# Kernel optimization log

Measured on AMD Instinct MI355X. Metric: run time of the kernel, lower is better.

The kernel has to match this reference:

```python
import jax, jax.numpy as jnp
import numpy as np

N = 100000
D = 128
E = 1600000
L = 3
LN_EPS = 1e-5
SM_EPS = 1e-16  # PyG softmax denominator eps
NEG_SLOPE = 0.2  # GATConv leaky_relu slope


def setup_inputs() -> dict:
    key = jax.random.key(0)
    ks = jax.random.split(key, 9)
    x = jax.random.normal(ks[0], (N, D), dtype=jnp.float32)
    edge_index = jax.random.randint(ks[1], (2, E), 0, N, dtype=jnp.int64)
    # Per-level GATConv params (heads=1, concat -> out dim D)
    W = jax.random.normal(ks[2], (L, D, D), dtype=jnp.float32) / np.sqrt(D)
    att_src = jax.random.normal(ks[3], (L, D), dtype=jnp.float32) / np.sqrt(D)
    att_dst = jax.random.normal(ks[4], (L, D), dtype=jnp.float32) / np.sqrt(D)
    bias = jnp.zeros((L, D), dtype=jnp.float32)
    ln_gamma = jnp.ones((L, D), dtype=jnp.float32)
    ln_beta = jnp.zeros((L, D), dtype=jnp.float32)
    return {"x": x, "edge_index": edge_index, "W": W, "att_src": att_src,
            "att_dst": att_dst, "bias": bias, "ln_gamma": ln_gamma, "ln_beta": ln_beta}


def _gat_level(x, src, dst, W, a_src, a_dst, b):
    h = x @ W                                   # [N, D] transformed features
    alpha_s = h @ a_src                         # [N] per-node src attention logit
    alpha_d = h @ a_dst                         # [N]
    alpha = alpha_s[src] + alpha_d[dst]         # [E'] edge logits
    alpha = jax.nn.leaky_relu(alpha, NEG_SLOPE)
    amax = jax.ops.segment_max(alpha, dst, num_segments=N)  # self-loops guarantee nonempty segments
    alpha = jnp.exp(alpha - amax[dst])
    denom = jax.ops.segment_sum(alpha, dst, num_segments=N)
    alpha = alpha / (denom[dst] + SM_EPS)       # segment softmax over incoming edges
    msg = h[src] * alpha[:, None]               # [E', D]
    out = jax.ops.segment_sum(msg, dst, num_segments=N)
    return out + b


def reference(x, edge_index, W, att_src, att_dst, bias, ln_gamma, ln_beta):
    loops = jnp.arange(N, dtype=edge_index.dtype)
    src = jnp.concatenate([edge_index[0], loops])  # PyG GATConv adds self-loops
    dst = jnp.concatenate([edge_index[1], loops])
    for i in range(L):
        x_att = _gat_level(x, src, dst, W[i], att_src[i], att_dst[i], bias[i])
        y = x + x_att
        mu = jnp.mean(y, axis=-1, keepdims=True)
        var = jnp.mean(jnp.square(y - mu), axis=-1, keepdims=True)
        y = (y - mu) * jax.lax.rsqrt(var + LN_EPS) * ln_gamma[i] + ln_beta[i]
        x = jax.nn.relu(y)  # dropout is identity in eval mode
    return x
```

## Files before the change

kernel.cpp:

```cpp
#include <hip/hip_runtime.h>
#include <hip/hip_fp16.h>
#include <cstdint>

#define D 128
#define NEG_SLOPE 0.2f
#define LN_EPS 1e-5f
#define SM_EPS 1e-16f

typedef _Float16 f16x8 __attribute__((ext_vector_type(8)));
typedef float f32x4 __attribute__((ext_vector_type(4)));


__global__ void hist_dst(const int* __restrict__ dst, int E, int* __restrict__ deg) {
    int e = blockIdx.x * blockDim.x + threadIdx.x;
    if (e < E) atomicAdd(&deg[dst[e]], 1);
}

__global__ void scanA(const int* __restrict__ deg, int n,
                      int* __restrict__ excl, int* __restrict__ bsums) {
    __shared__ int s[256];
    int t = threadIdx.x;
    int v = blockIdx.x * 256 + t;
    int d = (v < n) ? deg[v] : 0;
    s[t] = d;
    __syncthreads();
    for (int off = 1; off < 256; off <<= 1) {
        int tv = (t >= off) ? s[t - off] : 0;
        __syncthreads();
        s[t] += tv;
        __syncthreads();
    }
    if (v < n) excl[v] = s[t] - d;
    if (t == 255) bsums[blockIdx.x] = s[255];
}

__global__ void scanB(int* __restrict__ bsums, int nb) {
    __shared__ int s[512];
    int t = threadIdx.x;
    int v = (t < nb) ? bsums[t] : 0;
    s[t] = v;
    __syncthreads();
    for (int off = 1; off < 512; off <<= 1) {
        int tv = (t >= off) ? s[t - off] : 0;
        __syncthreads();
        s[t] += tv;
        __syncthreads();
    }
    if (t < nb) bsums[t] = s[t] - v;
}

__global__ void scanC(int* __restrict__ rowptr, const int* __restrict__ bsums,
                      int* __restrict__ cursor, int n, int total) {
    int v = blockIdx.x * blockDim.x + threadIdx.x;
    if (v < n) { rowptr[v] += bsums[v >> 8]; cursor[v] = 0; }
    if (v == 0) rowptr[n] = total;
}

__global__ void fill_csr(const int* __restrict__ src, const int* __restrict__ dst,
                         int E, const int* __restrict__ rowptr,
                         int* __restrict__ cursor, int* __restrict__ col) {
    int e = blockIdx.x * blockDim.x + threadIdx.x;
    if (e >= E) return;
    int d = dst[e];
    int p = rowptr[d] + atomicAdd(&cursor[d], 1);
    col[p] = src[e];
}


__global__ void prep_w(const float* __restrict__ W, const float* __restrict__ a_src,
                       const float* __restrict__ a_dst, __half* __restrict__ Wt,
                       float* __restrict__ wsv, float* __restrict__ wdv) {
    int l = blockIdx.x;
    const float* Wl = W + (size_t)l * D * D;
    __half* Wtl = Wt + (size_t)l * D * D;
    int t = threadIdx.x;
    __shared__ float sA[D], sD[D];
    if (t < D) { sA[t] = a_src[l * D + t]; sD[t] = a_dst[l * D + t]; }
    __syncthreads();
    if (t < D) {
        float ps = 0.f, pd = 0.f;
        for (int c = 0; c < D; ++c) {
            float wv = Wl[t * D + c];
            ps += wv * sA[c];
            pd += wv * sD[c];
        }
        wsv[l * D + t] = ps;
        wdv[l * D + t] = pd;
    }
    int c = t & 127, kh = t >> 7;
    for (int g = 0; g < 8; ++g) {
        int k0 = kh * 64 + g * 8;
        union { __half hv[8]; float4 f4; } u;
        #pragma unroll
        for (int rr = 0; rr < 8; ++rr) u.hv[rr] = __float2half(Wl[(k0 + rr) * D + c]);
        *(float4*)(Wtl + (size_t)c * D + k0) = u.f4;
    }
}


__global__ __launch_bounds__(256) void gemm_mfma(
        const float* __restrict__ x, const __half* __restrict__ Wt,
        const float* __restrict__ wsv, const float* __restrict__ wdv,
        __half* __restrict__ h, float* __restrict__ as_, float* __restrict__ ad_, int n) {
    __shared__ char sXa[32768];
    __shared__ char sWb[32768];
    int t = threadIdx.x;
    int row0 = blockIdx.x * 128;
    int lane = t & 63;
    int w = t >> 6;
    int wrow = (w >> 1) * 64;
    int wcol = (w & 1) * 64;

    const float4* xv = (const float4*)x;
    #pragma unroll
    for (int i = 0; i < 16; ++i) {
        int slot = i * 256 + t;
        int r = slot >> 5;
        int c4 = slot & 31;
        int gr = row0 + r;
        float4 v = (gr < n) ? xv[(size_t)gr * 32 + c4] : make_float4(0.f, 0.f, 0.f, 0.f);
        union { __half2 q[2]; float2 f; } u;
        u.q[0] = __floats2half2_rn(v.x, v.y);
        u.q[1] = __floats2half2_rn(v.z, v.w);
        *(float2*)(sXa + r * 256 + ((c4 * 8) ^ ((r & 7) << 4))) = u.f;
    }
    const float4* wv = (const float4*)Wt;
    #pragma unroll
    for (int i = 0; i < 8; ++i) {
        int chunk = i * 256 + t;
        int r = chunk >> 4;
        int c16 = chunk & 15;
        float4 v = wv[chunk];
        *(float4*)(sWb + r * 256 + ((c16 * 16) ^ ((r & 7) << 4))) = v;
    }
    __syncthreads();

    f32x4 acc[4][4];
    #pragma unroll
    for (int a = 0; a < 4; ++a)
        #pragma unroll
        for (int b = 0; b < 4; ++b) acc[a][b] = (f32x4){0.f, 0.f, 0.f, 0.f};

    #pragma unroll
    for (int ks = 0; ks < 4; ++ks) {
        int kbyte = ks * 64 + (lane >> 4) * 16;
        f16x8 aF[4], bF[4];
        #pragma unroll
        for (int tt = 0; tt < 4; ++tt) {
            int ra = wrow + tt * 16 + (lane & 15);
            aF[tt] = *(f16x8*)(sXa + ra * 256 + (kbyte ^ ((ra & 7) << 4)));
            int rb = wcol + tt * 16 + (lane & 15);
            bF[tt] = *(f16x8*)(sWb + rb * 256 + (kbyte ^ ((rb & 7) << 4)));
        }
        #pragma unroll
        for (int tr = 0; tr < 4; ++tr)
            #pragma unroll
            for (int tc = 0; tc < 4; ++tc)
                acc[tr][tc] = __builtin_amdgcn_mfma_f32_16x16x32_f16(aF[tr], bF[tc], acc[tr][tc], 0, 0, 0);
    }

    #pragma unroll
    for (int tr = 0; tr < 4; ++tr) {
        #pragma unroll
        for (int reg = 0; reg < 4; ++reg) {
            int gr = row0 + wrow + tr * 16 + (lane >> 4) * 4 + reg;
            if (gr < n) {
                #pragma unroll
                for (int tc = 0; tc < 4; ++tc) {
                    int gc = wcol + tc * 16 + (lane & 15);
                    h[(size_t)gr * D + gc] = __float2half(acc[tr][tc][reg]);
                }
            }
        }
    }

    int r = t >> 1, hh = t & 1;
    float ps = 0.f, pd = 0.f;
    const float4* s4 = (const float4*)wsv + hh * 16;
    const float4* d4 = (const float4*)wdv + hh * 16;
    #pragma unroll
    for (int g = 0; g < 8; ++g) {
        int kbyte = hh * 128 + g * 16;
        f16x8 xa = *(f16x8*)(sXa + r * 256 + (kbyte ^ ((r & 7) << 4)));
        float4 sa = s4[g * 2], sb = s4[g * 2 + 1];
        float4 da = d4[g * 2], db = d4[g * 2 + 1];
        ps += (float)xa[0] * sa.x + (float)xa[1] * sa.y + (float)xa[2] * sa.z + (float)xa[3] * sa.w
            + (float)xa[4] * sb.x + (float)xa[5] * sb.y + (float)xa[6] * sb.z + (float)xa[7] * sb.w;
        pd += (float)xa[0] * da.x + (float)xa[1] * da.y + (float)xa[2] * da.z + (float)xa[3] * da.w
            + (float)xa[4] * db.x + (float)xa[5] * db.y + (float)xa[6] * db.z + (float)xa[7] * db.w;
    }
    ps += __shfl_xor(ps, 1);
    pd += __shfl_xor(pd, 1);
    if (hh == 0 && row0 + r < n) { as_[row0 + r] = ps; ad_[row0 + r] = pd; }
}


__global__ __launch_bounds__(256) void aggregate(
        const float* __restrict__ xin, const __half* __restrict__ h,
        const float* __restrict__ as_, const float* __restrict__ ad_,
        const int* __restrict__ col, const int* __restrict__ rowptr,
        const float* __restrict__ bias, const float* __restrict__ gamma,
        const float* __restrict__ beta, float* __restrict__ xout, int n) {
    __shared__ int     sS[4][64];
    __shared__ __half2 sW[4][64];
    int tid = threadIdx.x;
    int wslot = tid >> 6;
    int lane = tid & 63;
    int wid = (int)((blockIdx.x * blockDim.x + tid) >> 6);
    if (wid >= n) return;
    int v = wid;
    int grp = lane >> 4;
    int gl  = lane & 15;
    int start = rowptr[v], end = rowptr[v + 1];
    float adv = ad_[v];
    float self_a = as_[v] + adv;
    self_a = (self_a > 0.f) ? self_a : NEG_SLOPE * self_a;

    float mval = self_a;
    int   s0 = 0;
    float a0 = -1e30f;
    for (int cb = start; cb < end; cb += 64) {
        int e = cb + lane;
        int   sl = 0;
        float al = -1e30f;
        if (e < end) {
            sl = col[e];
            float aa = as_[sl] + adv;
            al = (aa > 0.f) ? aa : NEG_SLOPE * aa;
        }
        if (cb == start) { s0 = sl; a0 = al; }
        mval = fmaxf(mval, al);
    }
    #pragma unroll
    for (int d = 32; d >= 1; d >>= 1) mval = fmaxf(mval, __shfl_xor(mval, d));

    float wl = __expf(a0 - mval);
    float sacc = wl;
    sS[wslot][lane] = s0;
    sW[wslot][lane] = __float2half2_rn(wl);

    __half2 hacc[4];
    #pragma unroll
    for (int j = 0; j < 4; ++j) hacc[j] = __float2half2_rn(0.f);

    const float4* h4 = (const float4*)h;

    for (int cb = start; cb < end; cb += 64) {
        if (cb != start) {
            int e = cb + lane;
            int   sl = 0;
            float al = -1e30f;
            if (e < end) {
                sl = col[e];
                float aa = as_[sl] + adv;
                al = (aa > 0.f) ? aa : NEG_SLOPE * aa;
            }
            float wl2 = __expf(al - mval);
            sacc += wl2;
            sS[wslot][lane] = sl;
            sW[wslot][lane] = __float2half2_rn(wl2);
        }
        int cnt = min(64, end - cb);
        for (int i = grp; i < cnt; i += 4) {
            int s = sS[wslot][i];
            __half2 w2 = sW[wslot][i];
            union { float4 f4; __half2 h2[4]; } u;
            u.f4 = h4[(size_t)s * 16 + gl];
            #pragma unroll
            for (int j = 0; j < 4; ++j) hacc[j] = __hfma2(u.h2[j], w2, hacc[j]);
        }
    }
    #pragma unroll
    for (int d = 32; d >= 1; d >>= 1) sacc += __shfl_xor(sacc, d);

    float acc[8];
    #pragma unroll
    for (int j = 0; j < 4; ++j) {
        float2 f = __half22float2(hacc[j]);
        acc[2 * j] = f.x;
        acc[2 * j + 1] = f.y;
    }
    #pragma unroll
    for (int j = 0; j < 8; ++j) {
        acc[j] += __shfl_xor(acc[j], 16);
        acc[j] += __shfl_xor(acc[j], 32);
    }

    float w_self = __expf(self_a - mval);
    sacc += w_self;
    {
        union { float4 f4; __half2 h2[4]; } u;
        u.f4 = h4[(size_t)v * 16 + gl];
        #pragma unroll
        for (int j = 0; j < 4; ++j) {
            float2 f = __half22float2(u.h2[j]);
            acc[2 * j]     += w_self * f.x;
            acc[2 * j + 1] += w_self * f.y;
        }
    }
    float inv = 1.f / (sacc + SM_EPS);

    const float4* xr = (const float4*)(xin + (size_t)v * D) + gl * 2;
    float4 xa = xr[0], xb = xr[1];
    const float4* b4 = (const float4*)bias + gl * 2;
    float4 ba = b4[0], bb = b4[1];
    float y[8];
    y[0] = xa.x + acc[0] * inv + ba.x;
    y[1] = xa.y + acc[1] * inv + ba.y;
    y[2] = xa.z + acc[2] * inv + ba.z;
    y[3] = xa.w + acc[3] * inv + ba.w;
    y[4] = xb.x + acc[4] * inv + bb.x;
    y[5] = xb.y + acc[5] * inv + bb.y;
    y[6] = xb.z + acc[6] * inv + bb.z;
    y[7] = xb.w + acc[7] * inv + bb.w;

    float s2 = 0.f;
    #pragma unroll
    for (int j = 0; j < 8; ++j) s2 += y[j];
    #pragma unroll
    for (int d = 8; d >= 1; d >>= 1) s2 += __shfl_xor(s2, d);
    float mu = s2 * (1.f / 128.f);
    float vs = 0.f;
    #pragma unroll
    for (int j = 0; j < 8; ++j) { float dd = y[j] - mu; vs += dd * dd; }
    #pragma unroll
    for (int d = 8; d >= 1; d >>= 1) vs += __shfl_xor(vs, d);
    float rstd = rsqrtf(vs * (1.f / 128.f) + LN_EPS);

    const float4* g4 = (const float4*)gamma + gl * 2;
    const float4* t4 = (const float4*)beta + gl * 2;
    float4 ga = g4[0], gb = g4[1];
    float4 ta = t4[0], tb = t4[1];
    float4 oa, ob;
    oa.x = fmaxf((y[0] - mu) * rstd * ga.x + ta.x, 0.f);
    oa.y = fmaxf((y[1] - mu) * rstd * ga.y + ta.y, 0.f);
    oa.z = fmaxf((y[2] - mu) * rstd * ga.z + ta.z, 0.f);
    oa.w = fmaxf((y[3] - mu) * rstd * ga.w + ta.w, 0.f);
    ob.x = fmaxf((y[4] - mu) * rstd * gb.x + tb.x, 0.f);
    ob.y = fmaxf((y[5] - mu) * rstd * gb.y + tb.y, 0.f);
    ob.z = fmaxf((y[6] - mu) * rstd * gb.z + tb.z, 0.f);
    ob.w = fmaxf((y[7] - mu) * rstd * gb.w + tb.w, 0.f);

    if (lane < 16) {
        float4* o4 = (float4*)(xout + (size_t)v * D) + gl * 2;
        o4[0] = oa;
        o4[1] = ob;
    }
}


extern "C" void kernel_launch(void* const* d_in, const int* in_sizes, int n_in,
                              void* d_out, int out_size, void* d_ws, size_t ws_size,
                              hipStream_t stream) {
    const float* x       = (const float*)d_in[0];
    const int*   edge    = (const int*)d_in[1];
    const float* W       = (const float*)d_in[2];
    const float* att_src = (const float*)d_in[3];
    const float* att_dst = (const float*)d_in[4];
    const float* bias    = (const float*)d_in[5];
    const float* gamma   = (const float*)d_in[6];
    const float* beta    = (const float*)d_in[7];
    float* out = (float*)d_out;

    const int N = in_sizes[0] / D;
    const int E = in_sizes[1] / 2;

    const int* src = edge;
    const int* dst = edge + E;

    char* ws = (char*)d_ws;
    size_t off = 0;
    auto carve = [&](size_t bytes) -> char* {
        char* p = ws + off;
        off = (off + bytes + 511) & ~(size_t)511;
        return p;
    };
    int*    rowptr = (int*)carve((size_t)(N + 1) * 4);
    int*    cursor = (int*)carve((size_t)N * 4);
    int*    bsums  = (int*)carve(512 * 4);
    int*    col    = (int*)carve((size_t)E * 4);
    __half* h      = (__half*)carve((size_t)N * D * 2);
    float*  as_    = (float*)carve((size_t)N * 4);
    float*  ad_    = (float*)carve((size_t)N * 4);
    float*  x1     = (float*)carve((size_t)N * D * 4);
    __half* Wt     = (__half*)carve((size_t)3 * D * D * 2);
    float*  wsv    = (float*)carve((size_t)3 * D * 4);
    float*  wdv    = (float*)carve((size_t)3 * D * 4);
    (void)ws_size;

    const int TPB = 256;
    int nbN = (N + TPB - 1) / TPB;
    int nbE = (E + TPB - 1) / TPB;

    prep_w<<<3, TPB, 0, stream>>>(W, att_src, att_dst, Wt, wsv, wdv);

    hipMemsetAsync(cursor, 0, (size_t)N * 4, stream);
    hist_dst<<<nbE, TPB, 0, stream>>>(dst, E, cursor);
    scanA<<<nbN, TPB, 0, stream>>>(cursor, N, rowptr, bsums);
    scanB<<<1, 512, 0, stream>>>(bsums, nbN);
    scanC<<<nbN, TPB, 0, stream>>>(rowptr, bsums, cursor, N, E);
    fill_csr<<<nbE, TPB, 0, stream>>>(src, dst, E, rowptr, cursor, col);

    int gemmGrid = (N + 127) / 128;
    int aggGrid  = (N * 64 + TPB - 1) / TPB;

    const float* xin = x;
    float* bufs[3] = { x1, x1, out };
    for (int l = 0; l < 3; ++l) {
        const __half* Wtl = Wt + (size_t)l * D * D;
        const float*  wsl = wsv + (size_t)l * D;
        const float*  wdl = wdv + (size_t)l * D;
        const float*  bl  = bias + (size_t)l * D;
        const float*  gl  = gamma + (size_t)l * D;
        const float*  btl = beta + (size_t)l * D;
        float* xout = bufs[l];

        gemm_mfma<<<gemmGrid, TPB, 0, stream>>>(xin, Wtl, wsl, wdl, h, as_, ad_, N);
        aggregate<<<aggGrid, TPB, 0, stream>>>(xin, h, as_, ad_, col, rowptr,
                                               bl, gl, btl, xout, N);
        xin = xout;
    }
}
```

Baseline: 626.3 us.

## Record per-edge rank in histogram pass and parallelize weight prep

```diff
diff --git a/kernel.cpp b/kernel.cpp
--- a/kernel.cpp
+++ b/kernel.cpp
@@ -11,9 +11,10 @@
 typedef float f32x4 __attribute__((ext_vector_type(4)));
 
 
-__global__ void hist_dst(const int* __restrict__ dst, int E, int* __restrict__ deg) {
+__global__ void hist_dst(const int* __restrict__ dst, int E,
+                         int* __restrict__ deg, int* __restrict__ rank) {
     int e = blockIdx.x * blockDim.x + threadIdx.x;
-    if (e < E) atomicAdd(&deg[dst[e]], 1);
+    if (e < E) rank[e] = atomicAdd(&deg[dst[e]], 1);
 }
 
 __global__ void scanA(const int* __restrict__ deg, int n,
@@ -50,50 +51,63 @@
 }
 
 __global__ void scanC(int* __restrict__ rowptr, const int* __restrict__ bsums,
-                      int* __restrict__ cursor, int n, int total) {
+                      int n, int total) {
     int v = blockIdx.x * blockDim.x + threadIdx.x;
-    if (v < n) { rowptr[v] += bsums[v >> 8]; cursor[v] = 0; }
+    if (v < n) rowptr[v] += bsums[v >> 8];
     if (v == 0) rowptr[n] = total;
 }
 
 __global__ void fill_csr(const int* __restrict__ src, const int* __restrict__ dst,
-                         int E, const int* __restrict__ rowptr,
-                         int* __restrict__ cursor, int* __restrict__ col) {
+                         const int* __restrict__ rank, int E,
+                         const int* __restrict__ rowptr, int* __restrict__ col) {
     int e = blockIdx.x * blockDim.x + threadIdx.x;
     if (e >= E) return;
     int d = dst[e];
-    int p = rowptr[d] + atomicAdd(&cursor[d], 1);
-    col[p] = src[e];
+    int p = rowptr[d] + rank[e];
+    atomicExch(&col[p], src[e]);
 }
 
 
 __global__ void prep_w(const float* __restrict__ W, const float* __restrict__ a_src,
                        const float* __restrict__ a_dst, __half* __restrict__ Wt,
                        float* __restrict__ wsv, float* __restrict__ wdv) {
-    int l = blockIdx.x;
+    int l = blockIdx.x >> 3;
+    int part = blockIdx.x & 7;
     const float* Wl = W + (size_t)l * D * D;
     __half* Wtl = Wt + (size_t)l * D * D;
     int t = threadIdx.x;
-    __shared__ float sA[D], sD[D];
-    if (t < D) { sA[t] = a_src[l * D + t]; sD[t] = a_dst[l * D + t]; }
+    int c0 = part * 16;
+
+    __shared__ float sT[128][17];
+    #pragma unroll
+    for (int i = 0; i < 8; ++i) {
+        int id = i * 256 + t;
+        int k = id >> 4, c = id & 15;
+        sT[k][c] = Wl[(size_t)k * D + c0 + c];
+    }
     __syncthreads();
-    if (t < D) {
-        float ps = 0.f, pd = 0.f;
-        for (int c = 0; c < D; ++c) {
-            float wv = Wl[t * D + c];
-            ps += wv * sA[c];
-            pd += wv * sD[c];
-        }
-        wsv[l * D + t] = ps;
-        wdv[l * D + t] = pd;
-    }
-    int c = t & 127, kh = t >> 7;
-    for (int g = 0; g < 8; ++g) {
-        int k0 = kh * 64 + g * 8;
+    {
+        int c = t >> 4, kg = t & 15;
         union { __half hv[8]; float4 f4; } u;
         #pragma unroll
-        for (int rr = 0; rr < 8; ++rr) u.hv[rr] = __float2half(Wl[(k0 + rr) * D + c]);
-        *(float4*)(Wtl + (size_t)c * D + k0) = u.f4;
+        for (int j = 0; j < 8; ++j) u.hv[j] = __float2half(sT[kg * 8 + j][c]);
+        *(float4*)(Wtl + (size_t)(c0 + c) * D + kg * 8) = u.f4;
+    }
+
+    if (part == 0) {
+        __shared__ float sA[D], sD[D];
+        if (t < D) { sA[t] = a_src[l * D + t]; sD[t] = a_dst[l * D + t]; }
+        __syncthreads();
+        if (t < D) {
+            float ps = 0.f, pd = 0.f;
+            for (int c = 0; c < D; ++c) {
+                float wv = Wl[(size_t)t * D + c];
+                ps += wv * sA[c];
+                pd += wv * sD[c];
+            }
+            wsv[l * D + t] = ps;
+            wdv[l * D + t] = pd;
+        }
     }
 }
 
@@ -376,9 +390,10 @@
         return p;
     };
     int*    rowptr = (int*)carve((size_t)(N + 1) * 4);
-    int*    cursor = (int*)carve((size_t)N * 4);
+    int*    deg    = (int*)carve((size_t)N * 4);
     int*    bsums  = (int*)carve(512 * 4);
     int*    col    = (int*)carve((size_t)E * 4);
+    int*    rank   = (int*)carve((size_t)E * 4);
     __half* h      = (__half*)carve((size_t)N * D * 2);
     float*  as_    = (float*)carve((size_t)N * 4);
     float*  ad_    = (float*)carve((size_t)N * 4);
@@ -392,14 +407,14 @@
     int nbN = (N + TPB - 1) / TPB;
     int nbE = (E + TPB - 1) / TPB;
 
-    prep_w<<<3, TPB, 0, stream>>>(W, att_src, att_dst, Wt, wsv, wdv);
-
-    hipMemsetAsync(cursor, 0, (size_t)N * 4, stream);
-    hist_dst<<<nbE, TPB, 0, stream>>>(dst, E, cursor);
-    scanA<<<nbN, TPB, 0, stream>>>(cursor, N, rowptr, bsums);
+    prep_w<<<24, TPB, 0, stream>>>(W, att_src, att_dst, Wt, wsv, wdv);
+
+    hipMemsetAsync(deg, 0, (size_t)N * 4, stream);
+    hist_dst<<<nbE, TPB, 0, stream>>>(dst, E, deg, rank);
+    scanA<<<nbN, TPB, 0, stream>>>(deg, N, rowptr, bsums);
     scanB<<<1, 512, 0, stream>>>(bsums, nbN);
-    scanC<<<nbN, TPB, 0, stream>>>(rowptr, bsums, cursor, N, E);
-    fill_csr<<<nbE, TPB, 0, stream>>>(src, dst, E, rowptr, cursor, col);
+    scanC<<<nbN, TPB, 0, stream>>>(rowptr, bsums, N, E);
+    fill_csr<<<nbE, TPB, 0, stream>>>(src, dst, rank, E, rowptr, col);
 
     int gemmGrid = (N + 127) / 128;
     int aggGrid  = (N * 64 + TPB - 1) / TPB;
```

After: 579.8 us. -7.4%, faster.
